# Optimization experiments

Measured on AMD Instinct MI355X. Metric: run time of the kernel, lower is better.

Reference implementation:

```python
import jax, jax.numpy as jnp
import numpy as np


def setup_inputs() -> dict:
    key = jax.random.key(0)
    ks = jax.random.split(key, 12)
    N, D = 150000, 100          # user_num + news_num nodes, emb_dim
    T, E, S = 16, 262144, 4096  # timesteps, edges/step, seeds/step
    CAT, K = 20, 9
    return {
        "node_emb": jax.random.normal(ks[0], (N, D), jnp.float32),
        "cx": jax.random.normal(ks[1], (N, D), jnp.float32),
        "rel_emb": jax.random.normal(ks[2], (CAT, D), jnp.float32),
        "W_ih": jax.random.normal(ks[3], (4 * D, D), jnp.float32) * 0.1,
        "W_hh": jax.random.normal(ks[4], (4 * D, D), jnp.float32) * 0.1,
        "b_ih": jax.random.normal(ks[5], (4 * D,), jnp.float32) * 0.1,
        "b_hh": jax.random.normal(ks[6], (4 * D,), jnp.float32) * 0.1,
        "src": jax.random.randint(ks[7], (T, E), 0, N, jnp.int64),
        "dst": jax.random.randint(ks[8], (T, E), 0, N, jnp.int64),
        "cat": jax.random.randint(ks[9], (T, E), 0, CAT, jnp.int64),
        "seeds": jax.random.randint(ks[10], (T, S), 0, 100000, jnp.int64),
        "cand_idx": jax.random.randint(ks[11], (T * S, K), 0, N, jnp.int64),
    }


def reference(node_emb, cx, rel_emb, W_ih, W_hh, b_ih, b_hh,
              src, dst, cat, seeds, cand_idx):
    N, D = node_emb.shape

    def step(carry, inputs):
        emb, c = carry
        s, d, ct, seed = inputs
        # previous hidden/cell state of seed users (before aggregation)
        h_prev = emb[seed]            # [S, D]
        c_prev = c[seed]              # [S, D]
        # edge-weighted gather-multiply-mean aggregation (send_and_recv)
        msg = emb[s] * rel_emb[ct]    # [E, D]
        agg = jax.ops.segment_sum(msg, d, num_segments=N)          # [N, D]
        cnt = jax.ops.segment_sum(jnp.ones(d.shape, emb.dtype), d,
                                  num_segments=N)                  # [N]
        emb = emb + agg / jnp.maximum(cnt, 1.0)[:, None]           # residual add
        # LSTMCell update on seed users
        x = emb[seed]                                              # [S, D]
        gates = x @ W_ih.T + b_ih + h_prev @ W_hh.T + b_hh         # [S, 4D]
        i_g, f_g, g_g, o_g = jnp.split(gates, 4, axis=-1)
        c_new = jax.nn.sigmoid(f_g) * c_prev + jax.nn.sigmoid(i_g) * jnp.tanh(g_g)
        h_new = jax.nn.sigmoid(o_g) * jnp.tanh(c_new)
        emb = emb.at[seed].set(h_new)
        c = c.at[seed].set(c_new)
        return (emb, c), h_new

    (emb_final, _), seed_embs = jax.lax.scan(
        step, (node_emb, cx), (src, dst, cat, seeds))
    # seed_embs: [T, S, D] -> per-click user embeddings
    user = seed_embs.reshape(-1, D)           # [T*S, D]
    cand = emb_final[cand_idx]                # [T*S, K, D]
    scores = jnp.einsum('nd,nkd->nk', user, cand)
    return scores
```

## Files before the change

### kernel.cpp

```cpp
#include <hip/hip_runtime.h>
#include <math.h>

#define N_NODES 150000
#define NODE_STRIDE 150016
#define DIM 100
#define D4 25
#define T_STEPS 16
#define E_EDGES 262144
#define S_SEEDS 4096
#define K_CAND 9
#define SPB 16
#define NPB 8

#define CB 64
#define BSPAN 2344
#define EPT 8
#define EPB (256 * EPT)
#define CBLK (E_EDGES / EPB)

__device__ __forceinline__ float sigmoidf_(float x) {
    return 1.0f / (1.0f + __expf(-x));
}


__global__ __launch_bounds__(256) void coarse_hist(
    const int* __restrict__ dst, int* __restrict__ bh) {
    int t = blockIdx.x / CBLK;
    int blk = blockIdx.x % CBLK;
    int base = t * E_EDGES + blk * EPB;
    int tid = threadIdx.x;
    __shared__ int h[CB];
    if (tid < CB) h[tid] = 0;
    __syncthreads();
#pragma unroll
    for (int e = 0; e < EPT; e++) {
        int d = dst[base + e * 256 + tid];
        atomicAdd(&h[d / BSPAN], 1);
    }
    __syncthreads();
    if (tid < CB) bh[(t * CBLK + blk) * CB + tid] = h[tid];
}

__global__ __launch_bounds__(64) void scan_bh(
    int* __restrict__ bh, int* __restrict__ coffs) {
    int t = blockIdx.x;
    int b = threadIdx.x;
    int run = 0;
    for (int blk = 0; blk < CBLK; blk++) {
        int idx = (t * CBLK + blk) * CB + b;
        int v = bh[idx];
        bh[idx] = run;
        run += v;
    }
    __shared__ int tot[CB];
    tot[b] = run;
    __syncthreads();
    if (b == 0) {
        int r = 0;
        for (int i = 0; i < CB; i++) { int c = tot[i]; tot[i] = r; r += c; }
    }
    __syncthreads();
    coffs[t * (CB + 1) + b] = tot[b];
    if (b == 0) coffs[t * (CB + 1) + CB] = E_EDGES;
}

__global__ __launch_bounds__(256) void coarse_scatter(
    const int* __restrict__ src, const int* __restrict__ dst,
    const int* __restrict__ cat, const int* __restrict__ bh,
    const int* __restrict__ coffs, int2* __restrict__ cbuf) {
    int t = blockIdx.x / CBLK;
    int blk = blockIdx.x % CBLK;
    int base = t * E_EDGES + blk * EPB;
    int tid = threadIdx.x;
    __shared__ int h[CB];
    __shared__ int gbase[CB];
    if (tid < CB) h[tid] = 0;
    __syncthreads();
    int rank[EPT], bb[EPT], dd[EPT];
#pragma unroll
    for (int e = 0; e < EPT; e++) {
        int d = dst[base + e * 256 + tid];
        int b = d / BSPAN;
        dd[e] = d; bb[e] = b;
        rank[e] = atomicAdd(&h[b], 1);
    }
    __syncthreads();
    if (tid < CB)
        gbase[tid] = coffs[t * (CB + 1) + tid] + bh[(t * CBLK + blk) * CB + tid];
    __syncthreads();
#pragma unroll
    for (int e = 0; e < EPT; e++) {
        int i = base + e * 256 + tid;
        int2 en;
        en.x = src[i] | (cat[i] << 18);
        en.y = dd[e];
        cbuf[(size_t)t * E_EDGES + gbase[bb[e]] + rank[e]] = en;
    }
}

__global__ __launch_bounds__(256) void fine_build(
    const int2* __restrict__ cbuf, const int* __restrict__ coffs,
    int4* __restrict__ meta, int* __restrict__ sorted) {
    int t = blockIdx.x >> 6;
    int b = blockIdx.x & 63;
    int node0 = b * BSPAN;
    int nodes = min(BSPAN, N_NODES - node0);
    int ebeg = coffs[t * (CB + 1) + b];
    int eend = coffs[t * (CB + 1) + b + 1];
    const int2* ebuf = cbuf + (size_t)t * E_EDGES;
    int4* mt = meta + (size_t)t * NODE_STRIDE;
    int* srt = sorted + (size_t)t * E_EDGES;
    __shared__ int cnt[BSPAN];
    __shared__ int begs[BSPAN];
    __shared__ int sums[256];
    int tid = threadIdx.x;

    for (int j = tid; j < BSPAN; j += 256) cnt[j] = 0;
    __syncthreads();
    for (int e = ebeg + tid; e < eend; e += 256)
        atomicAdd(&cnt[ebuf[e].y - node0], 1);
    __syncthreads();

    const int chunk = (BSPAN + 255) / 256;
    int cbeg = tid * chunk;
    int cend = min(cbeg + chunk, BSPAN);
    int s = 0;
    for (int j = cbeg; j < cend; j++) s += cnt[j];
    sums[tid] = s;
    __syncthreads();
    for (int d = 1; d < 256; d <<= 1) {
        int v = (tid >= d) ? sums[tid - d] : 0;
        __syncthreads();
        sums[tid] += v;
        __syncthreads();
    }
    int run = (tid == 0) ? 0 : sums[tid - 1];
    for (int j = cbeg; j < cend; j++) {
        int c = cnt[j];
        begs[j] = run;
        cnt[j] = run;
        run += c;
    }
    __syncthreads();

    for (int e = ebeg + tid; e < eend; e += 256) {
        int2 en = ebuf[e];
        int pos = atomicAdd(&cnt[en.y - node0], 1);
        srt[ebeg + pos] = en.x;
    }
    __syncthreads();

    for (int j = tid; j < nodes; j += 256) {
        int lbeg = begs[j];
        int deg = cnt[j] - lbeg;
        int gbeg = ebeg + lbeg;
        int4 m;
        m.x = gbeg | (deg << 19);
        m.y = (deg > 0) ? srt[gbeg] : 0;
        m.z = (deg > 1) ? srt[gbeg + 1] : 0;
        m.w = (deg > 2) ? srt[gbeg + 2] : 0;
        mt[node0 + j] = m;
    }
}

__global__ __launch_bounds__(256) void fused_agg(
    const float* __restrict__ emb_in, float* __restrict__ emb_out,
    const float* __restrict__ rel_emb, const int4* __restrict__ meta,
    const int* __restrict__ sorted) {
    int g = threadIdx.x >> 5;
    int lane = threadIdx.x & 31;
    int node = blockIdx.x * NPB + g;
    if (node >= N_NODES) return;
    bool act = lane < D4;
    float4 own = act ? ((const float4*)(emb_in + (size_t)node * DIM))[lane]
                     : make_float4(0.f, 0.f, 0.f, 0.f);
    int4 m = meta[node];
    int deg = ((unsigned)m.x) >> 19;
    int beg = m.x & 0x7FFFF;
    float4 acc = make_float4(0.f, 0.f, 0.f, 0.f);
    if (act) {
        if (deg > 0) {
            float4 mm = ((const float4*)(emb_in + (size_t)(m.y & 0x3FFFF) * DIM))[lane];
            float4 rr = ((const float4*)(rel_emb + (size_t)(m.y >> 18) * DIM))[lane];
            acc.x += mm.x * rr.x; acc.y += mm.y * rr.y;
            acc.z += mm.z * rr.z; acc.w += mm.w * rr.w;
        }
        if (deg > 1) {
            float4 mm = ((const float4*)(emb_in + (size_t)(m.z & 0x3FFFF) * DIM))[lane];
            float4 rr = ((const float4*)(rel_emb + (size_t)(m.z >> 18) * DIM))[lane];
            acc.x += mm.x * rr.x; acc.y += mm.y * rr.y;
            acc.z += mm.z * rr.z; acc.w += mm.w * rr.w;
        }
        if (deg > 2) {
            float4 mm = ((const float4*)(emb_in + (size_t)(m.w & 0x3FFFF) * DIM))[lane];
            float4 rr = ((const float4*)(rel_emb + (size_t)(m.w >> 18) * DIM))[lane];
            acc.x += mm.x * rr.x; acc.y += mm.y * rr.y;
            acc.z += mm.z * rr.z; acc.w += mm.w * rr.w;
        }
    }
    for (int e = beg + 3; e < beg + deg; e++) {
        int p = sorted[e];
        if (act) {
            float4 mm = ((const float4*)(emb_in + (size_t)(p & 0x3FFFF) * DIM))[lane];
            float4 rr = ((const float4*)(rel_emb + (size_t)(p >> 18) * DIM))[lane];
            acc.x += mm.x * rr.x; acc.y += mm.y * rr.y;
            acc.z += mm.z * rr.z; acc.w += mm.w * rr.w;
        }
    }
    if (act) {
        float inv = (deg > 0) ? 1.0f / (float)deg : 0.0f;
        own.x += acc.x * inv; own.y += acc.y * inv;
        own.z += acc.z * inv; own.w += acc.w * inv;
        ((float4*)(emb_out + (size_t)node * DIM))[lane] = own;
    }
}

__global__ __launch_bounds__(512) void lstm_kernel(
    const float* __restrict__ emb_new, const float* __restrict__ emb_old,
    const float* __restrict__ c_state, const int* __restrict__ seeds,
    const float* __restrict__ W_ih, const float* __restrict__ W_hh,
    const float* __restrict__ b_ih, const float* __restrict__ b_hh,
    float* __restrict__ h_out, float* __restrict__ c_out) {
    __shared__ __align__(16) float xs[SPB][DIM];
    __shared__ __align__(16) float hs[SPB][DIM];
    __shared__ __align__(16) float gates[SPB][4 * DIM];
    int tid = threadIdx.x;
    int base = blockIdx.x * SPB;

    for (int idx = tid; idx < SPB * D4; idx += 512) {
        int s = idx / D4, q = idx - s * D4;
        int node = seeds[base + s];
        ((float4*)xs[s])[q] = ((const float4*)(emb_new + (size_t)node * DIM))[q];
        ((float4*)hs[s])[q] = ((const float4*)(emb_old + (size_t)node * DIM))[q];
    }
    __syncthreads();

    if (tid < 4 * DIM) {
        int j = tid;
        float acc[SPB];
#pragma unroll
        for (int s = 0; s < SPB; s++) acc[s] = 0.0f;
        const float4* wi = (const float4*)(W_ih + (size_t)j * DIM);
        const float4* wh = (const float4*)(W_hh + (size_t)j * DIM);
        for (int dc = 0; dc < D4; dc++) {
            float4 a = wi[dc], b = wh[dc];
#pragma unroll
            for (int s = 0; s < SPB; s++) {
                float4 x = ((const float4*)xs[s])[dc];
                float4 h = ((const float4*)hs[s])[dc];
                acc[s] += x.x * a.x + x.y * a.y + x.z * a.z + x.w * a.w
                        + h.x * b.x + h.y * b.y + h.z * b.z + h.w * b.w;
            }
        }
        float bb = b_ih[j] + b_hh[j];
#pragma unroll
        for (int s = 0; s < SPB; s++) gates[s][j] = acc[s] + bb;
    }
    __syncthreads();

    for (int idx = tid; idx < SPB * D4; idx += 512) {
        int s = idx / D4, q = idx - s * D4;
        int node = seeds[base + s];
        float4 ig = ((const float4*)gates[s])[q];
        float4 fg = ((const float4*)(gates[s] + DIM))[q];
        float4 gg = ((const float4*)(gates[s] + 2 * DIM))[q];
        float4 og = ((const float4*)(gates[s] + 3 * DIM))[q];
        float4 cp = ((const float4*)(c_state + (size_t)node * DIM))[q];
        float4 cn, hn;
        cn.x = sigmoidf_(fg.x) * cp.x + sigmoidf_(ig.x) * tanhf(gg.x);
        cn.y = sigmoidf_(fg.y) * cp.y + sigmoidf_(ig.y) * tanhf(gg.y);
        cn.z = sigmoidf_(fg.z) * cp.z + sigmoidf_(ig.z) * tanhf(gg.z);
        cn.w = sigmoidf_(fg.w) * cp.w + sigmoidf_(ig.w) * tanhf(gg.w);
        hn.x = sigmoidf_(og.x) * tanhf(cn.x);
        hn.y = sigmoidf_(og.y) * tanhf(cn.y);
        hn.z = sigmoidf_(og.z) * tanhf(cn.z);
        hn.w = sigmoidf_(og.w) * tanhf(cn.w);
        ((float4*)(h_out + (size_t)(base + s) * DIM))[q] = hn;
        ((float4*)(c_out + (size_t)(base + s) * DIM))[q] = cn;
    }
}

__global__ __launch_bounds__(256) void scatter_seed(
    float* __restrict__ emb, float* __restrict__ c_state,
    const int* __restrict__ seeds,
    const float* __restrict__ h_new, const float* __restrict__ c_new) {
    int i = blockIdx.x * blockDim.x + threadIdx.x;
    int sd = i / D4, q = i - sd * D4;
    int node = seeds[sd];
    ((float4*)(emb + (size_t)node * DIM))[q] =
        ((const float4*)(h_new + (size_t)sd * DIM))[q];
    ((float4*)(c_state + (size_t)node * DIM))[q] =
        ((const float4*)(c_new + (size_t)sd * DIM))[q];
}

__global__ __launch_bounds__(64) void score_kernel(
    const float* __restrict__ seed_h, const float* __restrict__ emb,
    const int* __restrict__ cand_idx, float* __restrict__ out) {
    int n = blockIdx.x;
    int lane = threadIdx.x;
    float u0 = seed_h[(size_t)n * DIM + lane];
    float u1 = (lane + 64 < DIM) ? seed_h[(size_t)n * DIM + lane + 64] : 0.0f;
    for (int k = 0; k < K_CAND; k++) {
        int node = cand_idx[n * K_CAND + k];
        const float* ce = emb + (size_t)node * DIM;
        float p = u0 * ce[lane];
        if (lane + 64 < DIM) p += u1 * ce[lane + 64];
        for (int off = 32; off > 0; off >>= 1) p += __shfl_down(p, off);
        if (lane == 0) out[n * K_CAND + k] = p;
    }
}

extern "C" void kernel_launch(void* const* d_in, const int* in_sizes, int n_in,
                              void* d_out, int out_size, void* d_ws, size_t ws_size,
                              hipStream_t stream) {
    const float* node_emb = (const float*)d_in[0];
    const float* cx       = (const float*)d_in[1];
    const float* rel_emb  = (const float*)d_in[2];
    const float* W_ih     = (const float*)d_in[3];
    const float* W_hh     = (const float*)d_in[4];
    const float* b_ih     = (const float*)d_in[5];
    const float* b_hh     = (const float*)d_in[6];
    const int*   src      = (const int*)d_in[7];
    const int*   dst      = (const int*)d_in[8];
    const int*   cat      = (const int*)d_in[9];
    const int*   seeds    = (const int*)d_in[10];
    const int*   cand     = (const int*)d_in[11];
    float* out = (float*)d_out;

    char* wsb = (char*)d_ws;
    float* emb_a = (float*)wsb; wsb += sizeof(float) * (size_t)N_NODES * DIM;
    float* emb_b = (float*)wsb; wsb += sizeof(float) * (size_t)N_NODES * DIM;
    float* cst   = (float*)wsb; wsb += sizeof(float) * (size_t)N_NODES * DIM;
    float* cnew  = (float*)wsb; wsb += sizeof(float) * (size_t)S_SEEDS * DIM;
    float* seedh = (float*)wsb; wsb += sizeof(float) * (size_t)T_STEPS * S_SEEDS * DIM;
    int4* meta   = (int4*)wsb; wsb += sizeof(int4) * (size_t)T_STEPS * NODE_STRIDE;
    int* sorted  = (int*)wsb; wsb += sizeof(int) * (size_t)T_STEPS * E_EDGES;
    int* bh      = (int*)wsb; wsb += sizeof(int) * (size_t)T_STEPS * CBLK * CB;
    int* coffs   = (int*)wsb; wsb += sizeof(int) * T_STEPS * (CB + 1);
    int2* cbuf = (int2*)emb_b;

    coarse_hist<<<T_STEPS * CBLK, 256, 0, stream>>>(dst, bh);
    scan_bh<<<T_STEPS, 64, 0, stream>>>(bh, coffs);
    coarse_scatter<<<T_STEPS * CBLK, 256, 0, stream>>>(
        src, dst, cat, bh, coffs, cbuf);
    fine_build<<<T_STEPS * CB, 256, 0, stream>>>(cbuf, coffs, meta, sorted);

    hipMemcpyAsync(cst, cx, sizeof(float) * (size_t)N_NODES * DIM,
                   hipMemcpyDeviceToDevice, stream);

    const float* cur = node_emb;
    float* bufs[2] = {emb_b, emb_a};
    for (int t = 0; t < T_STEPS; t++) {
        float* nxt = bufs[t & 1];
        fused_agg<<<(N_NODES + NPB - 1) / NPB, 256, 0, stream>>>(
            cur, nxt, rel_emb,
            meta + (size_t)t * NODE_STRIDE, sorted + (size_t)t * E_EDGES);
        lstm_kernel<<<S_SEEDS / SPB, 512, 0, stream>>>(
            nxt, cur, cst, seeds + (size_t)t * S_SEEDS,
            W_ih, W_hh, b_ih, b_hh,
            seedh + (size_t)t * S_SEEDS * DIM, cnew);
        scatter_seed<<<(S_SEEDS * D4) / 256, 256, 0, stream>>>(
            nxt, cst, seeds + (size_t)t * S_SEEDS,
            seedh + (size_t)t * S_SEEDS * DIM, cnew);
        cur = nxt;
    }
    score_kernel<<<T_STEPS * S_SEEDS, 64, 0, stream>>>(seedh, cur, cand, out);
}
```

Measured before the change: 1.501 ms.

## Pack aggregation threads densely per node and batch candidate loads in scoring

The aggregation kernel now maps each thread to one float4 of a node's row (25 threads per node, packed contiguously) instead of 32-lane groups with 7 idle lanes, removing wasted threads and launching fewer blocks. Each thread loads the node metadata and walks the edge list independently, so degree-dependent loop divergence now occurs within wavefronts spanning multiple nodes. The score kernel preloads all candidate indices and issues all nine row loads before the reductions to increase memory-level parallelism.

```diff
diff --git a/kernel.cpp b/kernel.cpp
--- a/kernel.cpp
+++ b/kernel.cpp
@@ -10,7 +10,6 @@
 #define S_SEEDS 4096
 #define K_CAND 9
 #define SPB 16
-#define NPB 8
 
 #define CB 64
 #define BSPAN 2344
@@ -167,52 +166,44 @@
     const float* __restrict__ emb_in, float* __restrict__ emb_out,
     const float* __restrict__ rel_emb, const int4* __restrict__ meta,
     const int* __restrict__ sorted) {
-    int g = threadIdx.x >> 5;
-    int lane = threadIdx.x & 31;
-    int node = blockIdx.x * NPB + g;
+    unsigned idx = blockIdx.x * 256u + threadIdx.x;
+    unsigned node = idx / 25u;
+    unsigned q = idx - node * 25u;
     if (node >= N_NODES) return;
-    bool act = lane < D4;
-    float4 own = act ? ((const float4*)(emb_in + (size_t)node * DIM))[lane]
-                     : make_float4(0.f, 0.f, 0.f, 0.f);
+    float4 own = ((const float4*)(emb_in + (size_t)node * DIM))[q];
     int4 m = meta[node];
     int deg = ((unsigned)m.x) >> 19;
     int beg = m.x & 0x7FFFF;
     float4 acc = make_float4(0.f, 0.f, 0.f, 0.f);
-    if (act) {
-        if (deg > 0) {
-            float4 mm = ((const float4*)(emb_in + (size_t)(m.y & 0x3FFFF) * DIM))[lane];
-            float4 rr = ((const float4*)(rel_emb + (size_t)(m.y >> 18) * DIM))[lane];
-            acc.x += mm.x * rr.x; acc.y += mm.y * rr.y;
-            acc.z += mm.z * rr.z; acc.w += mm.w * rr.w;
-        }
-        if (deg > 1) {
-            float4 mm = ((const float4*)(emb_in + (size_t)(m.z & 0x3FFFF) * DIM))[lane];
-            float4 rr = ((const float4*)(rel_emb + (size_t)(m.z >> 18) * DIM))[lane];
-            acc.x += mm.x * rr.x; acc.y += mm.y * rr.y;
-            acc.z += mm.z * rr.z; acc.w += mm.w * rr.w;
-        }
-        if (deg > 2) {
-            float4 mm = ((const float4*)(emb_in + (size_t)(m.w & 0x3FFFF) * DIM))[lane];
-            float4 rr = ((const float4*)(rel_emb + (size_t)(m.w >> 18) * DIM))[lane];
-            acc.x += mm.x * rr.x; acc.y += mm.y * rr.y;
-            acc.z += mm.z * rr.z; acc.w += mm.w * rr.w;
-        }
+    if (deg > 0) {
+        float4 mm = ((const float4*)(emb_in + (size_t)(m.y & 0x3FFFF) * DIM))[q];
+        float4 rr = ((const float4*)(rel_emb + (size_t)(m.y >> 18) * DIM))[q];
+        acc.x += mm.x * rr.x; acc.y += mm.y * rr.y;
+        acc.z += mm.z * rr.z; acc.w += mm.w * rr.w;
+    }
+    if (deg > 1) {
+        float4 mm = ((const float4*)(emb_in + (size_t)(m.z & 0x3FFFF) * DIM))[q];
+        float4 rr = ((const float4*)(rel_emb + (size_t)(m.z >> 18) * DIM))[q];
+        acc.x += mm.x * rr.x; acc.y += mm.y * rr.y;
+        acc.z += mm.z * rr.z; acc.w += mm.w * rr.w;
+    }
+    if (deg > 2) {
+        float4 mm = ((const float4*)(emb_in + (size_t)(m.w & 0x3FFFF) * DIM))[q];
+        float4 rr = ((const float4*)(rel_emb + (size_t)(m.w >> 18) * DIM))[q];
+        acc.x += mm.x * rr.x; acc.y += mm.y * rr.y;
+        acc.z += mm.z * rr.z; acc.w += mm.w * rr.w;
     }
     for (int e = beg + 3; e < beg + deg; e++) {
         int p = sorted[e];
-        if (act) {
-            float4 mm = ((const float4*)(emb_in + (size_t)(p & 0x3FFFF) * DIM))[lane];
-            float4 rr = ((const float4*)(rel_emb + (size_t)(p >> 18) * DIM))[lane];
-            acc.x += mm.x * rr.x; acc.y += mm.y * rr.y;
-            acc.z += mm.z * rr.z; acc.w += mm.w * rr.w;
-        }
-    }
-    if (act) {
-        float inv = (deg > 0) ? 1.0f / (float)deg : 0.0f;
-        own.x += acc.x * inv; own.y += acc.y * inv;
-        own.z += acc.z * inv; own.w += acc.w * inv;
-        ((float4*)(emb_out + (size_t)node * DIM))[lane] = own;
-    }
+        float4 mm = ((const float4*)(emb_in + (size_t)(p & 0x3FFFF) * DIM))[q];
+        float4 rr = ((const float4*)(rel_emb + (size_t)(p >> 18) * DIM))[q];
+        acc.x += mm.x * rr.x; acc.y += mm.y * rr.y;
+        acc.z += mm.z * rr.z; acc.w += mm.w * rr.w;
+    }
+    float inv = (deg > 0) ? 1.0f / (float)deg : 0.0f;
+    own.x += acc.x * inv; own.y += acc.y * inv;
+    own.z += acc.z * inv; own.w += acc.w * inv;
+    ((float4*)(emb_out + (size_t)node * DIM))[q] = own;
 }
 
 __global__ __launch_bounds__(512) void lstm_kernel(
@@ -298,15 +289,24 @@
     const int* __restrict__ cand_idx, float* __restrict__ out) {
     int n = blockIdx.x;
     int lane = threadIdx.x;
+    bool hi = lane + 64 < DIM;
     float u0 = seed_h[(size_t)n * DIM + lane];
-    float u1 = (lane + 64 < DIM) ? seed_h[(size_t)n * DIM + lane + 64] : 0.0f;
+    float u1 = hi ? seed_h[(size_t)n * DIM + lane + 64] : 0.0f;
+    int cd[K_CAND];
+#pragma unroll
+    for (int k = 0; k < K_CAND; k++) cd[k] = cand_idx[n * K_CAND + k];
+    float p[K_CAND];
+#pragma unroll
     for (int k = 0; k < K_CAND; k++) {
-        int node = cand_idx[n * K_CAND + k];
-        const float* ce = emb + (size_t)node * DIM;
-        float p = u0 * ce[lane];
-        if (lane + 64 < DIM) p += u1 * ce[lane + 64];
-        for (int off = 32; off > 0; off >>= 1) p += __shfl_down(p, off);
-        if (lane == 0) out[n * K_CAND + k] = p;
+        const float* ce = emb + (size_t)cd[k] * DIM;
+        p[k] = u0 * ce[lane];
+        if (hi) p[k] += u1 * ce[lane + 64];
+    }
+#pragma unroll
+    for (int k = 0; k < K_CAND; k++) {
+        for (int off = 32; off > 0; off >>= 1)
+            p[k] += __shfl_down(p[k], off);
+        if (lane == 0) out[n * K_CAND + k] = p[k];
     }
 }
 
@@ -350,9 +350,10 @@
 
     const float* cur = node_emb;
     float* bufs[2] = {emb_b, emb_a};
+    const int agg_blocks = (N_NODES * D4 + 255) / 256;
     for (int t = 0; t < T_STEPS; t++) {
         float* nxt = bufs[t & 1];
-        fused_agg<<<(N_NODES + NPB - 1) / NPB, 256, 0, stream>>>(
+        fused_agg<<<agg_blocks, 256, 0, stream>>>(
             cur, nxt, rel_emb,
             meta + (size_t)t * NODE_STRIDE, sorted + (size_t)t * E_EDGES);
         lstm_kernel<<<S_SEEDS / SPB, 512, 0, stream>>>(
```

Result: no change. 1.517 ms (+1.1%).
